# Kernel optimization log

Measured on AMD Instinct MI355X. Metric: run time of the kernel, lower is better.

Reference implementation:

```python
import jax, jax.numpy as jnp
import numpy as np

NUM_NETS = 2_000_000
PINS_PER_NET = 4
NUM_PINS = NUM_NETS * PINS_PER_NET


def setup_inputs() -> dict:
    key = jax.random.key(0)
    k1, k2, k3 = jax.random.split(key, 3)
    num_slrX, num_slrY = 1, 4
    # pin positions already expressed in SLR-grid units: x in [0, num_slrX), y in [0, num_slrY)
    pos = jax.random.uniform(k1, (NUM_PINS, 2), jnp.float32) * jnp.array(
        [float(max(num_slrX, 1)), float(max(num_slrY, 1))], jnp.float32)
    # CSR netpin structure: each net owns PINS_PER_NET pins, flat list is a permutation of all pins
    flat_netpin = jax.random.permutation(k2, NUM_PINS).astype(jnp.int32)
    netpin_start = (jnp.arange(NUM_NETS + 1, dtype=jnp.int32) * PINS_PER_NET)
    net_ids = jnp.repeat(jnp.arange(NUM_NETS, dtype=jnp.int32), PINS_PER_NET)
    net_weights = jax.random.uniform(k3, (NUM_NETS,), jnp.float32, minval=0.5, maxval=1.5)
    net_mask = jnp.ones((NUM_NETS,), jnp.bool_)
    pin_mask = jnp.zeros((NUM_PINS,), jnp.bool_)
    inv_gamma = jnp.float32(2.0)  # 1 / gamma, gamma = 0.5
    return dict(pos=pos, flat_netpin=flat_netpin, netpin_start=netpin_start,
                net_ids=net_ids, net_weights=net_weights, net_mask=net_mask,
                pin_mask=pin_mask, inv_gamma=inv_gamma,
                num_slrX=num_slrX, num_slrY=num_slrY)


def reference(pos, flat_netpin, netpin_start, net_ids, net_weights, net_mask,
              pin_mask, inv_gamma, num_slrX, num_slrY):
    """Weighted-average SLL: per-net log-sum-exp weighted-average span of pin
    SLR coordinates, per dimension, counted only for dims with >1 SLR."""
    n = net_weights.shape[0]
    p = pos[flat_netpin]  # [P, 2] gather pin coords in CSR order
    # numerically-stable exp weights per net (segment max/min shift)
    mx = jax.ops.segment_max(p, net_ids, num_segments=n)  # [N, 2]
    mn = jax.ops.segment_min(p, net_ids, num_segments=n)  # [N, 2]
    ep = jnp.exp((p - mx[net_ids]) * inv_gamma)   # exp(+x/gamma), shifted
    en = jnp.exp((mn[net_ids] - p) * inv_gamma)   # exp(-x/gamma), shifted
    s_ep = jax.ops.segment_sum(ep, net_ids, num_segments=n)
    s_xep = jax.ops.segment_sum(p * ep, net_ids, num_segments=n)
    s_en = jax.ops.segment_sum(en, net_ids, num_segments=n)
    s_xen = jax.ops.segment_sum(p * en, net_ids, num_segments=n)
    wa = s_xep / s_ep - s_xen / s_en  # [N, 2] weighted-average span per dim
    dim_on = jnp.array([num_slrX > 1, num_slrY > 1], dtype=wa.dtype)  # only multi-SLR dims
    per_net = jnp.sum(wa * dim_on, axis=1)  # [N]
    return jnp.sum(jnp.where(net_mask, net_weights * per_net, jnp.float32(0.0)))
```

## Files before the change

kernel.cpp:

```cpp
#include <hip/hip_runtime.h>
#include <stdint.h>


#define PINB_SHIFT 13
#define PINB_SIZE  (1 << PINB_SHIFT)
#define MAX_PINB   1024
#define JB_SHIFT   14
#define JB_SIZE    (1 << JB_SHIFT)
#define MAX_JB     512
#define P1_CHUNK   8192
#define NTHR       1024

__device__ __forceinline__ float wa4(float a, float b, float c, float d, float ig) {
    float ea = __expf(a * ig), eb = __expf(b * ig);
    float ec = __expf(c * ig), ed = __expf(d * ig);
    float na = __expf(-a * ig), nb = __expf(-b * ig);
    float nc = __expf(-c * ig), nd = __expf(-d * ig);
    float s_ep  = ea + eb + ec + ed;
    float s_xep = a * ea + b * eb + c * ec + d * ed;
    float s_en  = na + nb + nc + nd;
    float s_xen = a * na + b * nb + c * nc + d * nd;
    return s_xep / s_ep - s_xen / s_en;
}

__global__ void init_kernel(unsigned* __restrict__ cur1, int n_pinb,
                            unsigned* __restrict__ cur2, int n_jb,
                            float* __restrict__ out) {
    int t = threadIdx.x;
    if (t == 0) out[0] = 0.0f;
    for (int i = t; i < n_pinb; i += blockDim.x) cur1[i] = (unsigned)i << PINB_SHIFT;
    for (int i = t; i < 2 * n_jb; i += blockDim.x) {
        int j = (i < n_jb) ? i : (i - n_jb);
        cur2[i] = (unsigned)j << JB_SHIFT;
    }
}

__global__ __launch_bounds__(NTHR) void p1_partition(
    const int4* __restrict__ fnp4, int NP, int n_pinb,
    uint2* __restrict__ ent1, unsigned* __restrict__ cur1)
{
    __shared__ uint2    staged[P1_CHUNK];
    __shared__ unsigned hist[MAX_PINB];
    __shared__ unsigned scn[MAX_PINB];
    __shared__ unsigned gbase[MAX_PINB];
    const int base  = blockIdx.x * P1_CHUNK;
    const int valid = min(P1_CHUNK, NP - base);
    const int t = threadIdx.x;

    for (int b = t; b < MAX_PINB; b += NTHR) hist[b] = 0;
    __syncthreads();

    unsigned pin[8], rnk[8];
    #pragma unroll
    for (int m4 = 0; m4 < 2; ++m4) {
        int k4 = t + NTHR * m4;
        int kk = 4 * k4;
        int4 v = make_int4(0, 0, 0, 0);
        if (kk < valid) v = fnp4[(base >> 2) + k4];
        pin[4*m4+0] = (unsigned)v.x; pin[4*m4+1] = (unsigned)v.y;
        pin[4*m4+2] = (unsigned)v.z; pin[4*m4+3] = (unsigned)v.w;
    }
    #pragma unroll
    for (int m4 = 0; m4 < 2; ++m4)
        #pragma unroll
        for (int c = 0; c < 4; ++c) {
            int kk = 4 * (t + NTHR * m4) + c;
            rnk[4*m4+c] = 0;
            if (kk < valid)
                rnk[4*m4+c] = atomicAdd(&hist[pin[4*m4+c] >> PINB_SHIFT], 1u);
        }
    __syncthreads();

    if (t < 64) {
        unsigned v[16], s = 0;
        #pragma unroll
        for (int i = 0; i < 16; ++i) { v[i] = hist[t * 16 + i]; s += v[i]; }
        unsigned e = s;
        #pragma unroll
        for (int off = 1; off < 64; off <<= 1) {
            unsigned u = __shfl_up(e, off, 64);
            if (t >= off) e += u;
        }
        e -= s;
        #pragma unroll
        for (int i = 0; i < 16; ++i) { scn[t * 16 + i] = e; e += v[i]; }
    }
    __syncthreads();

    for (int b = t; b < n_pinb; b += NTHR)
        if (hist[b]) gbase[b] = atomicAdd(&cur1[b], hist[b]);
    __syncthreads();

    #pragma unroll
    for (int m4 = 0; m4 < 2; ++m4)
        #pragma unroll
        for (int c = 0; c < 4; ++c) {
            int kk = 4 * (t + NTHR * m4) + c;
            if (kk < valid) {
                unsigned p = pin[4*m4+c];
                staged[scn[p >> PINB_SHIFT] + rnk[4*m4+c]] =
                    make_uint2(p, (unsigned)(base + kk));
            }
        }
    __syncthreads();

    for (int k = t; k < valid; k += NTHR) {
        uint2 e = staged[k];
        unsigned b = e.x >> PINB_SHIFT;
        ent1[gbase[b] + ((unsigned)k - scn[b])] = e;
    }
}

__global__ __launch_bounds__(NTHR) void p2_gather(
    const uint2* __restrict__ ent1, const float2* __restrict__ pos2,
    const int* __restrict__ slrx_p, const int* __restrict__ slry_p,
    int d, int NP, int n_jb,
    uint2* __restrict__ ent2, unsigned* __restrict__ cur2)
{
    const int slr = (d == 0) ? slrx_p[0] : slry_p[0];
    if (slr <= 1) return;

    __shared__ __align__(16) char smem[PINB_SIZE * sizeof(uint2) + 3 * MAX_JB * 4];
    float*    win    = (float*)smem;
    uint2*    staged = (uint2*)smem;
    unsigned* hist   = (unsigned*)(smem + PINB_SIZE * sizeof(uint2));
    unsigned* scn    = hist + MAX_JB;
    unsigned* gbase  = scn + MAX_JB;

    const int pbase = blockIdx.x << PINB_SHIFT;
    const int valid = min(PINB_SIZE, NP - pbase);
    const int t = threadIdx.x;

    uint2 e[8];
    #pragma unroll
    for (int m = 0; m < 8; ++m) {
        int k = t + NTHR * m;
        e[m] = make_uint2(0u, 0u);
        if (k < valid) e[m] = ent1[pbase + k];
    }
    for (int i = t; i < valid; i += NTHR) {
        float2 p = pos2[pbase + i];
        win[i] = d ? p.y : p.x;
    }
    if (t < MAX_JB) hist[t] = 0;
    __syncthreads();

    float yv[8]; unsigned rnk[8];
    #pragma unroll
    for (int m = 0; m < 8; ++m) {
        int k = t + NTHR * m;
        yv[m] = (k < valid) ? win[e[m].x & (PINB_SIZE - 1)] : 0.0f;
    }
    #pragma unroll
    for (int m = 0; m < 8; ++m) {
        int k = t + NTHR * m;
        rnk[m] = 0;
        if (k < valid) rnk[m] = atomicAdd(&hist[e[m].y >> JB_SHIFT], 1u);
    }
    __syncthreads();

    if (t < 64) {
        unsigned v[8], s = 0;
        #pragma unroll
        for (int i = 0; i < 8; ++i) { v[i] = hist[t * 8 + i]; s += v[i]; }
        unsigned ex = s;
        #pragma unroll
        for (int off = 1; off < 64; off <<= 1) {
            unsigned u = __shfl_up(ex, off, 64);
            if (t >= off) ex += u;
        }
        ex -= s;
        #pragma unroll
        for (int i = 0; i < 8; ++i) { scn[t * 8 + i] = ex; ex += v[i]; }
    }
    __syncthreads();

    for (int q = t; q < n_jb; q += NTHR)
        if (hist[q]) gbase[q] = atomicAdd(&cur2[q], hist[q]);
    __syncthreads();

    #pragma unroll
    for (int m = 0; m < 8; ++m) {
        int k = t + NTHR * m;
        if (k < valid)
            staged[scn[e[m].y >> JB_SHIFT] + rnk[m]] =
                make_uint2(e[m].y, __float_as_uint(yv[m]));
    }
    __syncthreads();

    for (int k = t; k < valid; k += NTHR) {
        uint2 s2 = staged[k];
        unsigned jb = s2.x >> JB_SHIFT;
        ent2[gbase[jb] + ((unsigned)k - scn[jb])] = s2;
    }
}

__global__ __launch_bounds__(NTHR) void p3_compute(
    const uint2* __restrict__ ent2, const float* __restrict__ wts,
    const float* __restrict__ ig_p,
    const int* __restrict__ slrx_p, const int* __restrict__ slry_p,
    int d, int NP, float* __restrict__ out)
{
    const int slr = (d == 0) ? slrx_p[0] : slry_p[0];
    if (slr <= 1) return;

    __shared__ float ytmp[JB_SIZE];
    const int jb     = blockIdx.x;
    const int base_j = jb << JB_SHIFT;
    const int nslots = min(JB_SIZE, NP - base_j);
    const int t = threadIdx.x;
    const float ig = ig_p[0];

    for (int k = t; k < nslots; k += NTHR) {
        uint2 e = ent2[base_j + k];
        ytmp[e.x & (JB_SIZE - 1)] = __uint_as_float(e.y);
    }
    __syncthreads();

    float val = 0.0f;
    const int nnets = nslots >> 2, bnet = base_j >> 2;
    const float4* y4 = (const float4*)ytmp;
    for (int i = t; i < nnets; i += NTHR) {
        float4 p = y4[i];
        val += wts[bnet + i] * wa4(p.x, p.y, p.z, p.w, ig);
    }

    #pragma unroll
    for (int off = 32; off > 0; off >>= 1) val += __shfl_down(val, off, 64);
    __syncthreads();
    if ((t & 63) == 0) ytmp[t >> 6] = val;
    __syncthreads();
    if (t == 0) {
        float s = 0.0f;
        #pragma unroll
        for (int w = 0; w < NTHR / 64; ++w) s += ytmp[w];
        atomicAdd(out, s);
    }
}

__global__ __launch_bounds__(256) void wasll_fallback(
    const float2* __restrict__ pos, const int4* __restrict__ fnp4,
    const float* __restrict__ net_weights, const float* __restrict__ inv_gamma_p,
    const int* __restrict__ slrx_p, const int* __restrict__ slry_p,
    float* __restrict__ out, int num_nets)
{
    const float ig = inv_gamma_p[0];
    const float dx = (slrx_p[0] > 1) ? 1.0f : 0.0f;
    const float dy = (slry_p[0] > 1) ? 1.0f : 0.0f;
    int net = blockIdx.x * blockDim.x + threadIdx.x;
    float val = 0.0f;
    if (net < num_nets) {
        int4 idx = fnp4[net];
        float2 p0 = pos[idx.x], p1 = pos[idx.y], p2 = pos[idx.z], p3 = pos[idx.w];
        val = net_weights[net] * (dx * wa4(p0.x, p1.x, p2.x, p3.x, ig)
                                + dy * wa4(p0.y, p1.y, p2.y, p3.y, ig));
    }
    #pragma unroll
    for (int off = 32; off > 0; off >>= 1) val += __shfl_down(val, off, 64);
    __shared__ float smem[4];
    if ((threadIdx.x & 63) == 0) smem[threadIdx.x >> 6] = val;
    __syncthreads();
    if (threadIdx.x == 0)
        atomicAdd(out, smem[0] + smem[1] + smem[2] + smem[3]);
}

__global__ void zero_out_kernel(float* __restrict__ out) { out[0] = 0.0f; }

extern "C" void kernel_launch(void* const* d_in, const int* in_sizes, int n_in,
                              void* d_out, int out_size, void* d_ws, size_t ws_size,
                              hipStream_t stream) {
    const float* posf        = (const float*)d_in[0];
    const int*   fnp         = (const int*)d_in[1];
    const float* net_weights = (const float*)d_in[4];
    const float* inv_gamma   = (const float*)d_in[7];
    const int*   slrx        = (const int*)d_in[8];
    const int*   slry        = (const int*)d_in[9];
    float*       out         = (float*)d_out;
    const int    N  = in_sizes[4];
    const int    NP = in_sizes[1];

    const int n_pinb = (NP + PINB_SIZE - 1) >> PINB_SHIFT;
    const int n_jb   = (NP + JB_SIZE - 1) >> JB_SHIFT;

    size_t off = 0;
    auto carve = [&](size_t bytes) { size_t o = off; off += (bytes + 255) & ~size_t(255); return o; };
    size_t o_ent1 = carve((size_t)n_pinb * PINB_SIZE * sizeof(uint2));
    size_t o_ent2 = carve((size_t)n_jb * JB_SIZE * sizeof(uint2));
    size_t o_cur1 = carve((size_t)n_pinb * sizeof(unsigned));
    size_t o_cur2 = carve((size_t)2 * n_jb * sizeof(unsigned));

    const bool ok = (NP == 4 * N) && (NP % 4 == 0) &&
                    (n_pinb <= MAX_PINB) && (n_jb <= MAX_JB) && (off <= ws_size);
    if (!ok) {
        hipLaunchKernelGGL(zero_out_kernel, dim3(1), dim3(1), 0, stream, out);
        const int block = 256, grid = (N + block - 1) / block;
        hipLaunchKernelGGL(wasll_fallback, dim3(grid), dim3(block), 0, stream,
                           (const float2*)posf, (const int4*)fnp, net_weights,
                           inv_gamma, slrx, slry, out, N);
        return;
    }

    char* ws = (char*)d_ws;
    uint2*    ent1 = (uint2*)(ws + o_ent1);
    uint2*    ent2 = (uint2*)(ws + o_ent2);
    unsigned* cur1 = (unsigned*)(ws + o_cur1);
    unsigned* cur2 = (unsigned*)(ws + o_cur2);

    hipLaunchKernelGGL(init_kernel, dim3(1), dim3(1024), 0, stream,
                       cur1, n_pinb, cur2, n_jb, out);

    const int g1 = (NP + P1_CHUNK - 1) / P1_CHUNK;
    hipLaunchKernelGGL(p1_partition, dim3(g1), dim3(NTHR), 0, stream,
                       (const int4*)fnp, NP, n_pinb, ent1, cur1);

    hipLaunchKernelGGL(p2_gather, dim3(n_pinb), dim3(NTHR), 0, stream,
                       ent1, (const float2*)posf, slrx, slry, 0, NP, n_jb, ent2, cur2);
    hipLaunchKernelGGL(p3_compute, dim3(n_jb), dim3(NTHR), 0, stream,
                       ent2, net_weights, inv_gamma, slrx, slry, 0, NP, out);

    hipLaunchKernelGGL(p2_gather, dim3(n_pinb), dim3(NTHR), 0, stream,
                       ent1, (const float2*)posf, slrx, slry, 1, NP, n_jb, ent2, cur2 + n_jb);
    hipLaunchKernelGGL(p3_compute, dim3(n_jb), dim3(NTHR), 0, stream,
                       ent2, net_weights, inv_gamma, slrx, slry, 1, NP, out);
}
```

Before: 274.0 us.

## Replace two-level bucket partitioning with inverse-permutation scatter and single fused eval

The shared-memory radix-style bucketing (partition, then per-dimension gather and compute passes) is replaced by three simple kernels. The first builds the inverse permutation of the netpin list with random 4-byte scatters. The second streams pin positions and scatters each active coordinate into CSR order. The third evaluates both dimensions per net in one pass. This removes the bucketing passes and the duplicated per-dimension launches, but the random global scatters rely on L2/MALL behaviour instead of coalesced bucketed writes.

```diff
diff --git a/kernel.cpp b/kernel.cpp
--- a/kernel.cpp
+++ b/kernel.cpp
@@ -2,14 +2,8 @@
 #include <stdint.h>
 
 
-#define PINB_SHIFT 13
-#define PINB_SIZE  (1 << PINB_SHIFT)
-#define MAX_PINB   1024
-#define JB_SHIFT   14
-#define JB_SIZE    (1 << JB_SHIFT)
-#define MAX_JB     512
-#define P1_CHUNK   8192
-#define NTHR       1024
+#define NTHR 1024
+#define GRID_CAP 2048
 
 __device__ __forceinline__ float wa4(float a, float b, float c, float d, float ig) {
     float ea = __expf(a * ig), eb = __expf(b * ig);
@@ -23,217 +17,85 @@
     return s_xep / s_ep - s_xen / s_en;
 }
 
-__global__ void init_kernel(unsigned* __restrict__ cur1, int n_pinb,
-                            unsigned* __restrict__ cur2, int n_jb,
-                            float* __restrict__ out) {
-    int t = threadIdx.x;
-    if (t == 0) out[0] = 0.0f;
-    for (int i = t; i < n_pinb; i += blockDim.x) cur1[i] = (unsigned)i << PINB_SHIFT;
-    for (int i = t; i < 2 * n_jb; i += blockDim.x) {
-        int j = (i < n_jb) ? i : (i - n_jb);
-        cur2[i] = (unsigned)j << JB_SHIFT;
+__global__ __launch_bounds__(NTHR) void p1_scatter(
+    const int4* __restrict__ fnp4, int NP4,
+    unsigned* __restrict__ inv, float* __restrict__ out)
+{
+    const int tid = blockIdx.x * blockDim.x + threadIdx.x;
+    if (tid == 0) out[0] = 0.0f;
+    const int stride = gridDim.x * blockDim.x;
+    for (int i = tid; i < NP4; i += stride) {
+        int4 v = fnp4[i];
+        unsigned k = (unsigned)(4 * i);
+        inv[(unsigned)v.x] = k;
+        inv[(unsigned)v.y] = k + 1;
+        inv[(unsigned)v.z] = k + 2;
+        inv[(unsigned)v.w] = k + 3;
     }
 }
 
-__global__ __launch_bounds__(NTHR) void p1_partition(
-    const int4* __restrict__ fnp4, int NP, int n_pinb,
-    uint2* __restrict__ ent1, unsigned* __restrict__ cur1)
+__global__ __launch_bounds__(NTHR) void p2_scatter(
+    const unsigned* __restrict__ inv, const float4* __restrict__ pos4,
+    const int* __restrict__ slrx_p, const int* __restrict__ slry_p,
+    int NP, float* __restrict__ e3x, float* __restrict__ e3y)
 {
-    __shared__ uint2    staged[P1_CHUNK];
-    __shared__ unsigned hist[MAX_PINB];
-    __shared__ unsigned scn[MAX_PINB];
-    __shared__ unsigned gbase[MAX_PINB];
-    const int base  = blockIdx.x * P1_CHUNK;
-    const int valid = min(P1_CHUNK, NP - base);
-    const int t = threadIdx.x;
-
-    for (int b = t; b < MAX_PINB; b += NTHR) hist[b] = 0;
-    __syncthreads();
-
-    unsigned pin[8], rnk[8];
-    #pragma unroll
-    for (int m4 = 0; m4 < 2; ++m4) {
-        int k4 = t + NTHR * m4;
-        int kk = 4 * k4;
-        int4 v = make_int4(0, 0, 0, 0);
-        if (kk < valid) v = fnp4[(base >> 2) + k4];
-        pin[4*m4+0] = (unsigned)v.x; pin[4*m4+1] = (unsigned)v.y;
-        pin[4*m4+2] = (unsigned)v.z; pin[4*m4+3] = (unsigned)v.w;
-    }
-    #pragma unroll
-    for (int m4 = 0; m4 < 2; ++m4)
-        #pragma unroll
-        for (int c = 0; c < 4; ++c) {
-            int kk = 4 * (t + NTHR * m4) + c;
-            rnk[4*m4+c] = 0;
-            if (kk < valid)
-                rnk[4*m4+c] = atomicAdd(&hist[pin[4*m4+c] >> PINB_SHIFT], 1u);
+    const bool dx = slrx_p[0] > 1, dy = slry_p[0] > 1;
+    if (!dx && !dy) return;
+    const unsigned np = (unsigned)NP;
+    const int tid = blockIdx.x * blockDim.x + threadIdx.x;
+    const int stride = gridDim.x * blockDim.x;
+    const int NP4 = NP >> 2;
+    const uint4* inv4 = (const uint4*)inv;
+    for (int i = tid; i < NP4; i += stride) {
+        uint4  kk = inv4[i];
+        float4 a  = pos4[2 * i];
+        float4 b  = pos4[2 * i + 1];
+        if (dy) {
+            if (kk.x < np) e3y[kk.x] = a.y;
+            if (kk.y < np) e3y[kk.y] = a.w;
+            if (kk.z < np) e3y[kk.z] = b.y;
+            if (kk.w < np) e3y[kk.w] = b.w;
         }
-    __syncthreads();
-
-    if (t < 64) {
-        unsigned v[16], s = 0;
-        #pragma unroll
-        for (int i = 0; i < 16; ++i) { v[i] = hist[t * 16 + i]; s += v[i]; }
-        unsigned e = s;
-        #pragma unroll
-        for (int off = 1; off < 64; off <<= 1) {
-            unsigned u = __shfl_up(e, off, 64);
-            if (t >= off) e += u;
+        if (dx) {
+            if (kk.x < np) e3x[kk.x] = a.x;
+            if (kk.y < np) e3x[kk.y] = a.z;
+            if (kk.z < np) e3x[kk.z] = b.x;
+            if (kk.w < np) e3x[kk.w] = b.z;
         }
-        e -= s;
-        #pragma unroll
-        for (int i = 0; i < 16; ++i) { scn[t * 16 + i] = e; e += v[i]; }
-    }
-    __syncthreads();
-
-    for (int b = t; b < n_pinb; b += NTHR)
-        if (hist[b]) gbase[b] = atomicAdd(&cur1[b], hist[b]);
-    __syncthreads();
-
-    #pragma unroll
-    for (int m4 = 0; m4 < 2; ++m4)
-        #pragma unroll
-        for (int c = 0; c < 4; ++c) {
-            int kk = 4 * (t + NTHR * m4) + c;
-            if (kk < valid) {
-                unsigned p = pin[4*m4+c];
-                staged[scn[p >> PINB_SHIFT] + rnk[4*m4+c]] =
-                    make_uint2(p, (unsigned)(base + kk));
-            }
-        }
-    __syncthreads();
-
-    for (int k = t; k < valid; k += NTHR) {
-        uint2 e = staged[k];
-        unsigned b = e.x >> PINB_SHIFT;
-        ent1[gbase[b] + ((unsigned)k - scn[b])] = e;
     }
 }
 
-__global__ __launch_bounds__(NTHR) void p2_gather(
-    const uint2* __restrict__ ent1, const float2* __restrict__ pos2,
+__global__ __launch_bounds__(NTHR) void p3_eval(
+    const float* __restrict__ e3x, const float* __restrict__ e3y,
+    const float* __restrict__ wts, const float* __restrict__ ig_p,
     const int* __restrict__ slrx_p, const int* __restrict__ slry_p,
-    int d, int NP, int n_jb,
-    uint2* __restrict__ ent2, unsigned* __restrict__ cur2)
+    int N, float* __restrict__ out)
 {
-    const int slr = (d == 0) ? slrx_p[0] : slry_p[0];
-    if (slr <= 1) return;
-
-    __shared__ __align__(16) char smem[PINB_SIZE * sizeof(uint2) + 3 * MAX_JB * 4];
-    float*    win    = (float*)smem;
-    uint2*    staged = (uint2*)smem;
-    unsigned* hist   = (unsigned*)(smem + PINB_SIZE * sizeof(uint2));
-    unsigned* scn    = hist + MAX_JB;
-    unsigned* gbase  = scn + MAX_JB;
-
-    const int pbase = blockIdx.x << PINB_SHIFT;
-    const int valid = min(PINB_SIZE, NP - pbase);
-    const int t = threadIdx.x;
-
-    uint2 e[8];
-    #pragma unroll
-    for (int m = 0; m < 8; ++m) {
-        int k = t + NTHR * m;
-        e[m] = make_uint2(0u, 0u);
-        if (k < valid) e[m] = ent1[pbase + k];
-    }
-    for (int i = t; i < valid; i += NTHR) {
-        float2 p = pos2[pbase + i];
-        win[i] = d ? p.y : p.x;
-    }
-    if (t < MAX_JB) hist[t] = 0;
-    __syncthreads();
-
-    float yv[8]; unsigned rnk[8];
-    #pragma unroll
-    for (int m = 0; m < 8; ++m) {
-        int k = t + NTHR * m;
-        yv[m] = (k < valid) ? win[e[m].x & (PINB_SIZE - 1)] : 0.0f;
-    }
-    #pragma unroll
-    for (int m = 0; m < 8; ++m) {
-        int k = t + NTHR * m;
-        rnk[m] = 0;
-        if (k < valid) rnk[m] = atomicAdd(&hist[e[m].y >> JB_SHIFT], 1u);
-    }
-    __syncthreads();
-
-    if (t < 64) {
-        unsigned v[8], s = 0;
-        #pragma unroll
-        for (int i = 0; i < 8; ++i) { v[i] = hist[t * 8 + i]; s += v[i]; }
-        unsigned ex = s;
-        #pragma unroll
-        for (int off = 1; off < 64; off <<= 1) {
-            unsigned u = __shfl_up(ex, off, 64);
-            if (t >= off) ex += u;
-        }
-        ex -= s;
-        #pragma unroll
-        for (int i = 0; i < 8; ++i) { scn[t * 8 + i] = ex; ex += v[i]; }
-    }
-    __syncthreads();
-
-    for (int q = t; q < n_jb; q += NTHR)
-        if (hist[q]) gbase[q] = atomicAdd(&cur2[q], hist[q]);
-    __syncthreads();
-
-    #pragma unroll
-    for (int m = 0; m < 8; ++m) {
-        int k = t + NTHR * m;
-        if (k < valid)
-            staged[scn[e[m].y >> JB_SHIFT] + rnk[m]] =
-                make_uint2(e[m].y, __float_as_uint(yv[m]));
-    }
-    __syncthreads();
-
-    for (int k = t; k < valid; k += NTHR) {
-        uint2 s2 = staged[k];
-        unsigned jb = s2.x >> JB_SHIFT;
-        ent2[gbase[jb] + ((unsigned)k - scn[jb])] = s2;
-    }
-}
-
-__global__ __launch_bounds__(NTHR) void p3_compute(
-    const uint2* __restrict__ ent2, const float* __restrict__ wts,
-    const float* __restrict__ ig_p,
-    const int* __restrict__ slrx_p, const int* __restrict__ slry_p,
-    int d, int NP, float* __restrict__ out)
-{
-    const int slr = (d == 0) ? slrx_p[0] : slry_p[0];
-    if (slr <= 1) return;
-
-    __shared__ float ytmp[JB_SIZE];
-    const int jb     = blockIdx.x;
-    const int base_j = jb << JB_SHIFT;
-    const int nslots = min(JB_SIZE, NP - base_j);
-    const int t = threadIdx.x;
+    const bool dx = slrx_p[0] > 1, dy = slry_p[0] > 1;
+    if (!dx && !dy) return;
     const float ig = ig_p[0];
-
-    for (int k = t; k < nslots; k += NTHR) {
-        uint2 e = ent2[base_j + k];
-        ytmp[e.x & (JB_SIZE - 1)] = __uint_as_float(e.y);
-    }
-    __syncthreads();
+    const int tid = blockIdx.x * blockDim.x + threadIdx.x;
+    const int stride = gridDim.x * blockDim.x;
+    const float4* x4 = (const float4*)e3x;
+    const float4* y4 = (const float4*)e3y;
 
     float val = 0.0f;
-    const int nnets = nslots >> 2, bnet = base_j >> 2;
-    const float4* y4 = (const float4*)ytmp;
-    for (int i = t; i < nnets; i += NTHR) {
-        float4 p = y4[i];
-        val += wts[bnet + i] * wa4(p.x, p.y, p.z, p.w, ig);
+    for (int j = tid; j < N; j += stride) {
+        float s = 0.0f;
+        if (dy) { float4 p = y4[j]; s += wa4(p.x, p.y, p.z, p.w, ig); }
+        if (dx) { float4 p = x4[j]; s += wa4(p.x, p.y, p.z, p.w, ig); }
+        val += wts[j] * s;
     }
 
     #pragma unroll
     for (int off = 32; off > 0; off >>= 1) val += __shfl_down(val, off, 64);
+    __shared__ float smem[NTHR / 64];
+    if ((threadIdx.x & 63) == 0) smem[threadIdx.x >> 6] = val;
     __syncthreads();
-    if ((t & 63) == 0) ytmp[t >> 6] = val;
-    __syncthreads();
-    if (t == 0) {
+    if (threadIdx.x == 0) {
         float s = 0.0f;
         #pragma unroll
-        for (int w = 0; w < NTHR / 64; ++w) s += ytmp[w];
+        for (int w = 0; w < NTHR / 64; ++w) s += smem[w];
         atomicAdd(out, s);
     }
 }
@@ -279,18 +141,13 @@
     const int    N  = in_sizes[4];
     const int    NP = in_sizes[1];
 
-    const int n_pinb = (NP + PINB_SIZE - 1) >> PINB_SHIFT;
-    const int n_jb   = (NP + JB_SIZE - 1) >> JB_SHIFT;
-
     size_t off = 0;
     auto carve = [&](size_t bytes) { size_t o = off; off += (bytes + 255) & ~size_t(255); return o; };
-    size_t o_ent1 = carve((size_t)n_pinb * PINB_SIZE * sizeof(uint2));
-    size_t o_ent2 = carve((size_t)n_jb * JB_SIZE * sizeof(uint2));
-    size_t o_cur1 = carve((size_t)n_pinb * sizeof(unsigned));
-    size_t o_cur2 = carve((size_t)2 * n_jb * sizeof(unsigned));
+    size_t o_inv = carve((size_t)NP * sizeof(unsigned));
+    size_t o_e3x = carve((size_t)NP * sizeof(float));
+    size_t o_e3y = carve((size_t)NP * sizeof(float));
 
-    const bool ok = (NP == 4 * N) && (NP % 4 == 0) &&
-                    (n_pinb <= MAX_PINB) && (n_jb <= MAX_JB) && (off <= ws_size);
+    const bool ok = (NP == 4 * N) && (NP % 4 == 0) && (off <= ws_size);
     if (!ok) {
         hipLaunchKernelGGL(zero_out_kernel, dim3(1), dim3(1), 0, stream, out);
         const int block = 256, grid = (N + block - 1) / block;
@@ -301,25 +158,18 @@
     }
 
     char* ws = (char*)d_ws;
-    uint2*    ent1 = (uint2*)(ws + o_ent1);
-    uint2*    ent2 = (uint2*)(ws + o_ent2);
-    unsigned* cur1 = (unsigned*)(ws + o_cur1);
-    unsigned* cur2 = (unsigned*)(ws + o_cur2);
+    unsigned* inv = (unsigned*)(ws + o_inv);
+    float*    e3x = (float*)(ws + o_e3x);
+    float*    e3y = (float*)(ws + o_e3y);
 
-    hipLaunchKernelGGL(init_kernel, dim3(1), dim3(1024), 0, stream,
-                       cur1, n_pinb, cur2, n_jb, out);
+    const int NP4 = NP >> 2;
+    int g12 = (NP4 + NTHR - 1) / NTHR; if (g12 > GRID_CAP) g12 = GRID_CAP;
+    int g3  = (N   + NTHR - 1) / NTHR; if (g3  > GRID_CAP) g3  = GRID_CAP;
 
-    const int g1 = (NP + P1_CHUNK - 1) / P1_CHUNK;
-    hipLaunchKernelGGL(p1_partition, dim3(g1), dim3(NTHR), 0, stream,
-                       (const int4*)fnp, NP, n_pinb, ent1, cur1);
-
-    hipLaunchKernelGGL(p2_gather, dim3(n_pinb), dim3(NTHR), 0, stream,
-                       ent1, (const float2*)posf, slrx, slry, 0, NP, n_jb, ent2, cur2);
-    hipLaunchKernelGGL(p3_compute, dim3(n_jb), dim3(NTHR), 0, stream,
-                       ent2, net_weights, inv_gamma, slrx, slry, 0, NP, out);
-
-    hipLaunchKernelGGL(p2_gather, dim3(n_pinb), dim3(NTHR), 0, stream,
-                       ent1, (const float2*)posf, slrx, slry, 1, NP, n_jb, ent2, cur2 + n_jb);
-    hipLaunchKernelGGL(p3_compute, dim3(n_jb), dim3(NTHR), 0, stream,
-                       ent2, net_weights, inv_gamma, slrx, slry, 1, NP, out);
+    hipLaunchKernelGGL(p1_scatter, dim3(g12), dim3(NTHR), 0, stream,
+                       (const int4*)fnp, NP4, inv, out);
+    hipLaunchKernelGGL(p2_scatter, dim3(g12), dim3(NTHR), 0, stream,
+                       inv, (const float4*)posf, slrx, slry, NP, e3x, e3y);
+    hipLaunchKernelGGL(p3_eval, dim3(g3), dim3(NTHR), 0, stream,
+                       e3x, e3y, net_weights, inv_gamma, slrx, slry, N, out);
 }
```

After: 446.0 us. 1.63x slower.
